# Kernel tuning notes

Measured on AMD Instinct MI355X. Metric: run time of the kernel, lower is better.

## Reference

```python
import jax, jax.numpy as jnp
import numpy as np

N_NODES = 50000
N_EDGES = 800000
D_IN, D_HID, D_OUT = 256, 128, 64
NEG_SLOPE = 0.2  # PyG GATConv default


def gat_conv(x, W, a_src, a_dst, b, src, dst, n):
    """Single-head PyG-style GATConv with self-loops already in (src, dst)."""
    h = x @ W                                  # [N, d_out]
    # per-edge attention logits: LeakyReLU(a_src . h_src + a_dst . h_dst)
    e = jax.nn.leaky_relu((h @ a_src)[src] + (h @ a_dst)[dst], NEG_SLOPE)  # [E]
    # segment softmax over incoming edges of each dst node (stable)
    e = e - jax.ops.segment_max(e, dst, num_segments=n)[dst]
    p = jnp.exp(e)
    p = p / jax.ops.segment_sum(p, dst, num_segments=n)[dst]
    # weighted scatter-add of source messages
    out = jax.ops.segment_sum(p[:, None] * h[src], dst, num_segments=n)
    return out + b


def setup_inputs() -> dict:
    key = jax.random.key(0)
    ks = jax.random.split(key, 10)
    x = jax.random.normal(ks[0], (N_NODES, D_IN), dtype=jnp.float32)
    edge_index = jax.random.randint(ks[1], (2, N_EDGES), 0, N_NODES, dtype=jnp.int32)
    s1 = 1.0 / np.sqrt(D_IN)
    s2 = 1.0 / np.sqrt(D_HID)
    W1 = jax.random.normal(ks[2], (D_IN, D_HID), dtype=jnp.float32) * s1
    a_src1 = jax.random.normal(ks[3], (D_HID,), dtype=jnp.float32) * s2
    a_dst1 = jax.random.normal(ks[4], (D_HID,), dtype=jnp.float32) * s2
    b1 = jnp.zeros((D_HID,), dtype=jnp.float32)
    W2 = jax.random.normal(ks[5], (D_HID, D_OUT), dtype=jnp.float32) * s2
    a_src2 = jax.random.normal(ks[6], (D_OUT,), dtype=jnp.float32) * (1.0 / np.sqrt(D_OUT))
    a_dst2 = jax.random.normal(ks[7], (D_OUT,), dtype=jnp.float32) * (1.0 / np.sqrt(D_OUT))
    b2 = jnp.zeros((D_OUT,), dtype=jnp.float32)
    return {"x": x, "edge_index": edge_index, "W1": W1, "a_src1": a_src1,
            "a_dst1": a_dst1, "b1": b1, "W2": W2, "a_src2": a_src2,
            "a_dst2": a_dst2, "b2": b2}


def reference(x, edge_index, W1, a_src1, a_dst1, b1, W2, a_src2, a_dst2, b2):
    n = x.shape[0]
    loops = jnp.arange(n, dtype=edge_index.dtype)
    src = jnp.concatenate([edge_index[0], loops])  # add_self_loops=True (PyG default)
    dst = jnp.concatenate([edge_index[1], loops])
    h = gat_conv(x, W1, a_src1, a_dst1, b1, src, dst, n)
    h = jax.nn.relu(h)
    return gat_conv(h, W2, a_src2, a_dst2, b2, src, dst, n)
```

## Files before the change

kernel.cpp:

```cpp
#include <hip/hip_runtime.h>
#include <stdint.h>

#define DIN 256
#define DHID 128
#define DOUTD 64
#define NBLK 128
#define BCAP 4096
#define SCAP 1024

typedef __attribute__((ext_vector_type(8))) short bf16x8;
typedef __attribute__((ext_vector_type(4))) float f32x4;

__device__ __forceinline__ uint32_t pack_bf16x2(float x, float y) {
    uint32_t ux = __builtin_bit_cast(uint32_t, x);
    uint32_t uy = __builtin_bit_cast(uint32_t, y);
    ux += 0x7fffu + ((ux >> 16) & 1u);
    uy += 0x7fffu + ((uy >> 16) & 1u);
    return (ux >> 16) | (uy & 0xffff0000u);
}
__device__ __forceinline__ uint16_t to_bf16(float x) {
    uint32_t u = __builtin_bit_cast(uint32_t, x);
    u += 0x7fffu + ((u >> 16) & 1u);
    return (uint16_t)(u >> 16);
}
__device__ __forceinline__ float bflo(uint32_t v) { return __builtin_bit_cast(float, v << 16); }
__device__ __forceinline__ float bfhi(uint32_t v) { return __builtin_bit_cast(float, v & 0xffff0000u); }

template<int K, int N>
__device__ __forceinline__ void prepack_body(
    const float* __restrict__ W, uint16_t* __restrict__ Bp, int t)
{
    constexpr int CB = N / 16;
    if (t >= (K / 32) * CB * 64) return;
    const int lane = t & 63, fi = t >> 6;
    const int c = fi % CB, kb = fi / CB;
    const int j  = 16 * c + (lane & 15);
    const int k0 = kb * 32 + (lane >> 4) * 8;
    uint32_t o[4];
    #pragma unroll
    for (int i = 0; i < 4; ++i) {
        float lo = W[(size_t)(k0 + 2 * i)     * N + j];
        float hi = W[(size_t)(k0 + 2 * i + 1) * N + j];
        o[i] = pack_bf16x2(lo, hi);
    }
    *reinterpret_cast<uint4*>(&Bp[(size_t)t * 8]) = make_uint4(o[0], o[1], o[2], o[3]);
}

__global__ __launch_bounds__(256) void prepack_both_kernel(
    const float* __restrict__ W1, uint16_t* __restrict__ Bp1,
    const float* __restrict__ W2, uint16_t* __restrict__ Bp2,
    int* __restrict__ cntG, int nbuck)
{
    if (blockIdx.x == 0) {
        for (int i = threadIdx.x; i < nbuck; i += 256) cntG[i] = 0;
    }
    if (blockIdx.x < 16)
        prepack_body<DIN, DHID>(W1, Bp1, blockIdx.x * 256 + threadIdx.x);
    else
        prepack_body<DHID, DOUTD>(W2, Bp2, (blockIdx.x - 16) * 256 + threadIdx.x);
}

template<int K, int N, bool AF32>
__device__ __forceinline__ void gemm_body(
    uint16_t* __restrict__ As,
    const void* __restrict__ A, const uint16_t* __restrict__ Bp,
    uint16_t* __restrict__ Cout, const float* __restrict__ a_s,
    const float* __restrict__ a_d, float* __restrict__ asrc,
    float* __restrict__ adst, int M, int bid)
{
    constexpr int KB = K / 32, CB = N / 16;
    const int tid = threadIdx.x;
    const int row0 = bid * 64;

    if (AF32) {
        constexpr int NIT = 64 * K / 4 / 256;
        #pragma unroll
        for (int i = 0; i < NIT; ++i) {
            int u = tid + i * 256;
            int row = u / (K / 4);
            int k4  = (u % (K / 4)) * 4;
            float4 v = make_float4(0.f, 0.f, 0.f, 0.f);
            if (row0 + row < M)
                v = *reinterpret_cast<const float4*>((const float*)A + (size_t)(row0 + row) * K + k4);
            uint32_t byte = (uint32_t)row * (K * 2) + k4 * 2;
            byte ^= (row & 7) << 4;
            *reinterpret_cast<uint2*>((char*)As + byte) =
                make_uint2(pack_bf16x2(v.x, v.y), pack_bf16x2(v.z, v.w));
        }
    } else {
        constexpr int NIT = 64 * K / 8 / 256;
        #pragma unroll
        for (int i = 0; i < NIT; ++i) {
            int u = tid + i * 256;
            int row = u / (K / 8);
            int k8  = (u % (K / 8)) * 8;
            uint4 v = make_uint4(0u, 0u, 0u, 0u);
            if (row0 + row < M)
                v = *reinterpret_cast<const uint4*>((const uint16_t*)A + (size_t)(row0 + row) * K + k8);
            uint32_t byte = (uint32_t)row * (K * 2) + k8 * 2;
            byte ^= (row & 7) << 4;
            *reinterpret_cast<uint4*>((char*)As + byte) = v;
        }
    }
    __syncthreads();

    const int w = tid >> 6, l = tid & 63;
    const int rA = w * 16 + (l & 15);

    f32x4 acc[CB] = {};
    const char* blane = (const char*)Bp + l * 16;

    #pragma unroll
    for (int kb = 0; kb < KB; ++kb) {
        uint32_t abyte = (uint32_t)rA * (K * 2) + (kb * 32 + (l >> 4) * 8) * 2;
        abyte ^= (rA & 7) << 4;
        bf16x8 a = *reinterpret_cast<const bf16x8*>((const char*)As + abyte);
        #pragma unroll
        for (int c = 0; c < CB; ++c) {
            bf16x8 b = *reinterpret_cast<const bf16x8*>(blane + (size_t)(kb * CB + c) * 1024);
            acc[c] = __builtin_amdgcn_mfma_f32_16x16x32_bf16(a, b, acc[c], 0, 0, 0);
        }
    }

    const int rb = w * 16 + (l >> 4) * 4;
    const int colb = l & 15;

    #pragma unroll
    for (int c = 0; c < CB; ++c) {
        #pragma unroll
        for (int r = 0; r < 4; ++r) {
            int grow = row0 + rb + r;
            if (grow < M)
                Cout[(size_t)grow * N + c * 16 + colb] = to_bf16(acc[c][r]);
        }
    }

    float ps[4] = {}, pd[4] = {};
    #pragma unroll
    for (int c = 0; c < CB; ++c) {
        float asv = a_s[c * 16 + colb];
        float adv = a_d[c * 16 + colb];
        #pragma unroll
        for (int r = 0; r < 4; ++r) {
            ps[r] += acc[c][r] * asv;
            pd[r] += acc[c][r] * adv;
        }
    }
    #pragma unroll
    for (int mask = 1; mask < 16; mask <<= 1) {
        #pragma unroll
        for (int r = 0; r < 4; ++r) {
            ps[r] += __shfl_xor(ps[r], mask);
            pd[r] += __shfl_xor(pd[r], mask);
        }
    }
    if (colb == 0) {
        #pragma unroll
        for (int r = 0; r < 4; ++r) {
            int grow = row0 + rb + r;
            if (grow < M) { asrc[grow] = ps[r]; adst[grow] = pd[r]; }
        }
    }
}

__global__ __launch_bounds__(256) void hybrid_kernel(
    const int* __restrict__ ei, int E, int n, int nbuck, int chunk,
    int* __restrict__ cntG, uint32_t* __restrict__ bucketed,
    const float* __restrict__ x, const uint16_t* __restrict__ Bp1,
    uint16_t* __restrict__ Hb, const float* __restrict__ a_s,
    const float* __restrict__ a_d, float* __restrict__ asrc,
    float* __restrict__ adst)
{
    __shared__ __align__(16) uint16_t As[64 * DIN];
    __shared__ int h[512];
    __shared__ int curL[512];

    if (blockIdx.x < NBLK) {
        for (int i = threadIdx.x; i < nbuck; i += 256) h[i] = 0;
        __syncthreads();
        const int blk = blockIdx.x;
        const int ET = E + n;
        const int e0 = blk * chunk, e1 = min(e0 + chunk, ET);
        for (int e = e0 + threadIdx.x; e < e1; e += 256) {
            int d = (e < E) ? ei[E + e] : (e - E);
            atomicAdd(&h[d >> 7], 1);
        }
        __syncthreads();
        for (int i = threadIdx.x; i < nbuck; i += 256) {
            int c = h[i];
            int base = i * BCAP;
            if (c) base += atomicAdd(&cntG[i], c);
            curL[i] = base;
        }
        __syncthreads();
        for (int e = e0 + threadIdx.x; e < e1; e += 256) {
            int s, d;
            if (e < E) { s = ei[e]; d = ei[E + e]; }
            else       { s = e - E; d = s; }
            int pos = atomicAdd(&curL[d >> 7], 1);
            bucketed[pos] = ((uint32_t)d << 16) | (uint32_t)s;
        }
    } else {
        gemm_body<DIN, DHID, true>(As, x, Bp1, Hb, a_s, a_d, asrc, adst, n,
                                   blockIdx.x - NBLK);
    }
}

__global__ __launch_bounds__(256) void gemm2_kernel(
    const uint16_t* __restrict__ A, const uint16_t* __restrict__ Bp,
    uint16_t* __restrict__ Cout, const float* __restrict__ a_s,
    const float* __restrict__ a_d, float* __restrict__ asrc,
    float* __restrict__ adst, int M)
{
    __shared__ __align__(16) uint16_t As[64 * DHID];
    gemm_body<DHID, DOUTD, false>(As, A, Bp, Cout, a_s, a_d, asrc, adst, M,
                                  blockIdx.x);
}

template<int D, bool RELU, bool OUTB16>
__global__ __launch_bounds__(256) void aggF_kernel(
    const uint32_t* __restrict__ bucketed, const int* __restrict__ cntG,
    const uint32_t* __restrict__ Hb, const float* __restrict__ asrc,
    const float* __restrict__ adst, const float* __restrict__ bias,
    void* __restrict__ out, int n)
{
    constexpr int C16 = D / 8;
    constexpr int EPI = 64 / C16;
    __shared__ uint16_t csr_l[SCAP];
    __shared__ int hist[32];
    __shared__ int scn[32];
    __shared__ int offs_l[32];
    __shared__ int cur[32];

    const int b     = blockIdx.x >> 2;
    const int slice = blockIdx.x & 3;
    const int tid = threadIdx.x;
    const int bbase = b * BCAP;
    const int cnt = cntG[b];

    if (tid < 32) hist[tid] = 0;
    __syncthreads();
    for (int i = tid; i < cnt; i += 256) {
        uint32_t pk = bucketed[bbase + i];
        int ln = (pk >> 16) & 127;
        if ((ln >> 5) == slice) atomicAdd(&hist[ln & 31], 1);
    }
    __syncthreads();
    if (tid < 32) scn[tid] = hist[tid];
    __syncthreads();
    #pragma unroll
    for (int off = 1; off < 32; off <<= 1) {
        int v = (tid < 32 && tid >= off) ? scn[tid - off] : 0;
        __syncthreads();
        if (tid < 32) scn[tid] += v;
        __syncthreads();
    }
    if (tid < 32) {
        int excl = scn[tid] - hist[tid];
        offs_l[tid] = excl;
        cur[tid] = excl;
    }
    __syncthreads();
    for (int i = tid; i < cnt; i += 256) {
        uint32_t pk = bucketed[bbase + i];
        int ln = (pk >> 16) & 127;
        if ((ln >> 5) == slice) {
            int pos = atomicAdd(&cur[ln & 31], 1);
            csr_l[pos] = (uint16_t)(pk & 0xFFFFu);
        }
    }
    __syncthreads();

    const int wv = tid >> 6, lane = tid & 63;
    const int seg = lane / C16;
    const int chk = lane & (C16 - 1);
    const uint4* __restrict__ H4 = reinterpret_cast<const uint4*>(Hb);

    for (int j = 0; j < 8; ++j) {
        const int ln = wv + 4 * j;
        const int node = b * 128 + slice * 32 + ln;
        if (node >= n) continue;
        const int beg = offs_l[ln];
        const int deg = hist[ln];
        const float ad = adst[node];

        float acc[8] = {};
        float ssum = 0.f;

        for (int base = 0; base < deg; base += 64) {
            const int lim = min(64, deg - base);
            float wt = 0.f; int st = 0;
            if (lane < lim) {
                st = csr_l[beg + base + lane];
                float t = asrc[st] + ad;
                t = (t > 0.f) ? t : 0.2f * t;
                wt = __expf(t);
            }
            ssum += wt;
            const int iters = (lim + 2 * EPI - 1) / (2 * EPI);
            #pragma unroll 2
            for (int it = 0; it < iters; ++it) {
                int e0 = it * 2 * EPI + seg;
                int e1 = e0 + EPI;
                float w0 = __shfl(wt, e0);
                int   s0 = __shfl(st, e0);
                float w1 = __shfl(wt, e1);
                int   s1 = __shfl(st, e1);
                uint4 v0 = H4[(size_t)s0 * (D / 8) + chk];
                uint4 v1 = H4[(size_t)s1 * (D / 8) + chk];
                acc[0] += w0 * bflo(v0.x); acc[1] += w0 * bfhi(v0.x);
                acc[2] += w0 * bflo(v0.y); acc[3] += w0 * bfhi(v0.y);
                acc[4] += w0 * bflo(v0.z); acc[5] += w0 * bfhi(v0.z);
                acc[6] += w0 * bflo(v0.w); acc[7] += w0 * bfhi(v0.w);
                acc[0] += w1 * bflo(v1.x); acc[1] += w1 * bfhi(v1.x);
                acc[2] += w1 * bflo(v1.y); acc[3] += w1 * bfhi(v1.y);
                acc[4] += w1 * bflo(v1.z); acc[5] += w1 * bfhi(v1.z);
                acc[6] += w1 * bflo(v1.w); acc[7] += w1 * bfhi(v1.w);
            }
        }

        #pragma unroll
        for (int mask = C16; mask < 64; mask <<= 1)
            #pragma unroll
            for (int q = 0; q < 8; ++q)
                acc[q] += __shfl_xor(acc[q], mask);
        #pragma unroll
        for (int off = 32; off; off >>= 1) ssum += __shfl_xor(ssum, off);
        const float inv = 1.f / ssum;

        if (seg == 0) {
            const int col0 = chk * 8;
            float r[8];
            #pragma unroll
            for (int q = 0; q < 8; ++q) {
                r[q] = acc[q] * inv + bias[col0 + q];
                if (RELU) r[q] = fmaxf(r[q], 0.f);
            }
            if (OUTB16) {
                uint4 o = make_uint4(pack_bf16x2(r[0], r[1]), pack_bf16x2(r[2], r[3]),
                                     pack_bf16x2(r[4], r[5]), pack_bf16x2(r[6], r[7]));
                *(reinterpret_cast<uint4*>(out) + (size_t)node * (D / 8) + chk) = o;
            } else {
                float* op = (float*)out + (size_t)node * D + col0;
                *reinterpret_cast<float4*>(op)     = make_float4(r[0], r[1], r[2], r[3]);
                *reinterpret_cast<float4*>(op + 4) = make_float4(r[4], r[5], r[6], r[7]);
            }
        }
    }
}

extern "C" void kernel_launch(void* const* d_in, const int* in_sizes, int n_in,
                              void* d_out, int out_size, void* d_ws, size_t ws_size,
                              hipStream_t stream)
{
    const float* x   = (const float*)d_in[0];
    const int*   ei  = (const int*)  d_in[1];
    const float* W1  = (const float*)d_in[2];
    const float* as1 = (const float*)d_in[3];
    const float* ad1 = (const float*)d_in[4];
    const float* b1  = (const float*)d_in[5];
    const float* W2  = (const float*)d_in[6];
    const float* as2 = (const float*)d_in[7];
    const float* ad2 = (const float*)d_in[8];
    const float* b2  = (const float*)d_in[9];
    float* out = (float*)d_out;

    const int n  = in_sizes[0] / DIN;
    const int E  = in_sizes[1] / 2;
    const int ET = E + n;

    const int nbuck  = (n + 127) >> 7;
    const int chunk  = (ET + NBLK - 1) / NBLK;

    char* ws = (char*)d_ws;
    size_t off = 0;
    auto alloc = [&](size_t bytes) -> void* {
        off = (off + 255) & ~(size_t)255;
        void* p = ws + off;
        off += bytes;
        return p;
    };
    uint16_t* Hb   = (uint16_t*)alloc((size_t)n * DHID * 2);
    uint16_t* O1b  = (uint16_t*)alloc((size_t)n * DHID * 2);
    uint16_t* H2b  = (uint16_t*)alloc((size_t)n * DOUTD * 2);
    float* asrc    = (float*)alloc((size_t)n * 4);
    float* adst    = (float*)alloc((size_t)n * 4);
    uint16_t* Bp1  = (uint16_t*)alloc((size_t)DIN * DHID * 2);
    uint16_t* Bp2  = (uint16_t*)alloc((size_t)DHID * DOUTD * 2);
    int* cntG  = (int*)alloc((size_t)nbuck * 4);
    uint32_t* bucketed = (uint32_t*)alloc((size_t)nbuck * BCAP * 4);

    const int ng = (n + 63) / 64;

    prepack_both_kernel<<<20, 256, 0, stream>>>(W1, Bp1, W2, Bp2, cntG, nbuck);

    hybrid_kernel<<<NBLK + ng, 256, 0, stream>>>(
        ei, E, n, nbuck, chunk, cntG, bucketed,
        x, Bp1, Hb, as1, ad1, asrc, adst);

    aggF_kernel<DHID, true, true><<<nbuck * 4, 256, 0, stream>>>(
        bucketed, cntG, (const uint32_t*)Hb, asrc, adst, b1, O1b, n);

    gemm2_kernel<<<ng, 256, 0, stream>>>(O1b, Bp2, H2b, as2, ad2, asrc, adst, n);

    aggF_kernel<DOUTD, false, false><<<nbuck * 4, 256, 0, stream>>>(
        bucketed, cntG, (const uint32_t*)H2b, asrc, adst, b2, out, n);
}
```

Before: 209.2 us.

## Fuse layer-2 GEMM into layer-1 aggregation and split hybrid bucketing/GEMM kernel

Layer-1 aggregation now keeps each block's 32 output rows in swizzled shared memory and runs the layer-2 MFMA GEMM and attention-logit projection in the same kernel. This removes the O1 intermediate round trip through global memory and one kernel launch. The former hybrid kernel, which ran edge bucketing and GEMM1 in one grid, is split into two separate sequential kernels, so the two phases no longer overlap. Layer-2 logits also get their own buffers.

```diff
diff --git a/kernel.cpp b/kernel.cpp
--- a/kernel.cpp
+++ b/kernel.cpp
@@ -163,67 +163,246 @@
     }
 }
 
-__global__ __launch_bounds__(256) void hybrid_kernel(
-    const int* __restrict__ ei, int E, int n, int nbuck, int chunk,
-    int* __restrict__ cntG, uint32_t* __restrict__ bucketed,
-    const float* __restrict__ x, const uint16_t* __restrict__ Bp1,
-    uint16_t* __restrict__ Hb, const float* __restrict__ a_s,
-    const float* __restrict__ a_d, float* __restrict__ asrc,
-    float* __restrict__ adst)
-{
-    __shared__ __align__(16) uint16_t As[64 * DIN];
-    __shared__ int h[512];
-    __shared__ int curL[512];
-
-    if (blockIdx.x < NBLK) {
-        for (int i = threadIdx.x; i < nbuck; i += 256) h[i] = 0;
-        __syncthreads();
-        const int blk = blockIdx.x;
-        const int ET = E + n;
-        const int e0 = blk * chunk, e1 = min(e0 + chunk, ET);
-        for (int e = e0 + threadIdx.x; e < e1; e += 256) {
-            int d = (e < E) ? ei[E + e] : (e - E);
-            atomicAdd(&h[d >> 7], 1);
-        }
-        __syncthreads();
-        for (int i = threadIdx.x; i < nbuck; i += 256) {
-            int c = h[i];
-            int base = i * BCAP;
-            if (c) base += atomicAdd(&cntG[i], c);
-            curL[i] = base;
-        }
-        __syncthreads();
-        for (int e = e0 + threadIdx.x; e < e1; e += 256) {
-            int s, d;
-            if (e < E) { s = ei[e]; d = ei[E + e]; }
-            else       { s = e - E; d = s; }
-            int pos = atomicAdd(&curL[d >> 7], 1);
-            bucketed[pos] = ((uint32_t)d << 16) | (uint32_t)s;
-        }
-    } else {
-        gemm_body<DIN, DHID, true>(As, x, Bp1, Hb, a_s, a_d, asrc, adst, n,
-                                   blockIdx.x - NBLK);
-    }
-}
-
-__global__ __launch_bounds__(256) void gemm2_kernel(
-    const uint16_t* __restrict__ A, const uint16_t* __restrict__ Bp,
+__global__ __launch_bounds__(256) void gemm1_kernel(
+    const float* __restrict__ A, const uint16_t* __restrict__ Bp,
     uint16_t* __restrict__ Cout, const float* __restrict__ a_s,
     const float* __restrict__ a_d, float* __restrict__ asrc,
     float* __restrict__ adst, int M)
 {
-    __shared__ __align__(16) uint16_t As[64 * DHID];
-    gemm_body<DHID, DOUTD, false>(As, A, Bp, Cout, a_s, a_d, asrc, adst, M,
-                                  blockIdx.x);
-}
-
-template<int D, bool RELU, bool OUTB16>
-__global__ __launch_bounds__(256) void aggF_kernel(
+    __shared__ __align__(16) uint16_t As[64 * DIN];
+    gemm_body<DIN, DHID, true>(As, A, Bp, Cout, a_s, a_d, asrc, adst, M, blockIdx.x);
+}
+
+__global__ __launch_bounds__(256) void histscatter_kernel(
+    const int* __restrict__ ei, int E, int n, int nbuck, int chunk,
+    int* __restrict__ cntG, uint32_t* __restrict__ bucketed)
+{
+    __shared__ int h[512];
+    __shared__ int curL[512];
+    for (int i = threadIdx.x; i < nbuck; i += 256) h[i] = 0;
+    __syncthreads();
+    const int blk = blockIdx.x;
+    const int ET = E + n;
+    const int e0 = blk * chunk, e1 = min(e0 + chunk, ET);
+    for (int e = e0 + threadIdx.x; e < e1; e += 256) {
+        int d = (e < E) ? ei[E + e] : (e - E);
+        atomicAdd(&h[d >> 7], 1);
+    }
+    __syncthreads();
+    for (int i = threadIdx.x; i < nbuck; i += 256) {
+        int c = h[i];
+        int base = i * BCAP;
+        if (c) base += atomicAdd(&cntG[i], c);
+        curL[i] = base;
+    }
+    __syncthreads();
+    for (int e = e0 + threadIdx.x; e < e1; e += 256) {
+        int s, d;
+        if (e < E) { s = ei[e]; d = ei[E + e]; }
+        else       { s = e - E; d = s; }
+        int pos = atomicAdd(&curL[d >> 7], 1);
+        bucketed[pos] = ((uint32_t)d << 16) | (uint32_t)s;
+    }
+}
+
+__global__ __launch_bounds__(256) void aggF1_fused_kernel(
+    const uint32_t* __restrict__ bucketed, const int* __restrict__ cntG,
+    const uint32_t* __restrict__ Hb, const float* __restrict__ asrc1,
+    const float* __restrict__ adst1, const float* __restrict__ b1,
+    const uint16_t* __restrict__ Bp2, const float* __restrict__ as2,
+    const float* __restrict__ ad2, uint16_t* __restrict__ H2b,
+    float* __restrict__ asrc2, float* __restrict__ adst2, int n)
+{
+    constexpr int C16 = DHID / 8;
+    constexpr int EPI = 64 / C16;
+    __shared__ uint16_t csr_l[SCAP];
+    __shared__ int hist[32];
+    __shared__ int scn[32];
+    __shared__ int offs_l[32];
+    __shared__ int cur[32];
+    __shared__ __align__(16) uint16_t O1[32 * DHID];
+    __shared__ float ps_l[32][2], pd_l[32][2];
+
+    const int b     = blockIdx.x >> 2;
+    const int slice = blockIdx.x & 3;
+    const int tid = threadIdx.x;
+    const int bbase = b * BCAP;
+    const int cnt = cntG[b];
+    const int nodebase = b * 128 + slice * 32;
+
+    if (tid < 32) hist[tid] = 0;
+    __syncthreads();
+    for (int i = tid; i < cnt; i += 256) {
+        uint32_t pk = bucketed[bbase + i];
+        int ln = (pk >> 16) & 127;
+        if ((ln >> 5) == slice) atomicAdd(&hist[ln & 31], 1);
+    }
+    __syncthreads();
+    if (tid < 32) scn[tid] = hist[tid];
+    __syncthreads();
+    #pragma unroll
+    for (int off = 1; off < 32; off <<= 1) {
+        int v = (tid < 32 && tid >= off) ? scn[tid - off] : 0;
+        __syncthreads();
+        if (tid < 32) scn[tid] += v;
+        __syncthreads();
+    }
+    if (tid < 32) {
+        int excl = scn[tid] - hist[tid];
+        offs_l[tid] = excl;
+        cur[tid] = excl;
+    }
+    __syncthreads();
+    for (int i = tid; i < cnt; i += 256) {
+        uint32_t pk = bucketed[bbase + i];
+        int ln = (pk >> 16) & 127;
+        if ((ln >> 5) == slice) {
+            int pos = atomicAdd(&cur[ln & 31], 1);
+            csr_l[pos] = (uint16_t)(pk & 0xFFFFu);
+        }
+    }
+    __syncthreads();
+
+    const int wv = tid >> 6, lane = tid & 63;
+    const int seg = lane / C16;
+    const int chk = lane & (C16 - 1);
+    const uint4* __restrict__ H4 = reinterpret_cast<const uint4*>(Hb);
+
+    for (int j = 0; j < 8; ++j) {
+        const int ln = wv + 4 * j;
+        const int node = nodebase + ln;
+        float acc[8] = {};
+        float ssum = 0.f;
+        if (node < n) {
+            const int beg = offs_l[ln];
+            const int deg = hist[ln];
+            const float ad = adst1[node];
+            for (int base = 0; base < deg; base += 64) {
+                const int lim = min(64, deg - base);
+                float wt = 0.f; int st = 0;
+                if (lane < lim) {
+                    st = csr_l[beg + base + lane];
+                    float t = asrc1[st] + ad;
+                    t = (t > 0.f) ? t : 0.2f * t;
+                    wt = __expf(t);
+                }
+                ssum += wt;
+                const int iters = (lim + 2 * EPI - 1) / (2 * EPI);
+                #pragma unroll 2
+                for (int it = 0; it < iters; ++it) {
+                    int e0 = it * 2 * EPI + seg;
+                    int e1 = e0 + EPI;
+                    float w0 = __shfl(wt, e0);
+                    int   s0 = __shfl(st, e0);
+                    float w1 = __shfl(wt, e1);
+                    int   s1 = __shfl(st, e1);
+                    uint4 v0 = H4[(size_t)s0 * C16 + chk];
+                    uint4 v1 = H4[(size_t)s1 * C16 + chk];
+                    acc[0] += w0 * bflo(v0.x); acc[1] += w0 * bfhi(v0.x);
+                    acc[2] += w0 * bflo(v0.y); acc[3] += w0 * bfhi(v0.y);
+                    acc[4] += w0 * bflo(v0.z); acc[5] += w0 * bfhi(v0.z);
+                    acc[6] += w0 * bflo(v0.w); acc[7] += w0 * bfhi(v0.w);
+                    acc[0] += w1 * bflo(v1.x); acc[1] += w1 * bfhi(v1.x);
+                    acc[2] += w1 * bflo(v1.y); acc[3] += w1 * bfhi(v1.y);
+                    acc[4] += w1 * bflo(v1.z); acc[5] += w1 * bfhi(v1.z);
+                    acc[6] += w1 * bflo(v1.w); acc[7] += w1 * bfhi(v1.w);
+                }
+            }
+            #pragma unroll
+            for (int mask = C16; mask < 64; mask <<= 1)
+                #pragma unroll
+                for (int q = 0; q < 8; ++q)
+                    acc[q] += __shfl_xor(acc[q], mask);
+            #pragma unroll
+            for (int off = 32; off; off >>= 1) ssum += __shfl_xor(ssum, off);
+        }
+        if (seg == 0) {
+            uint4 o = make_uint4(0u, 0u, 0u, 0u);
+            if (node < n) {
+                const float inv = 1.f / ssum;
+                const int col0 = chk * 8;
+                float r[8];
+                #pragma unroll
+                for (int q = 0; q < 8; ++q)
+                    r[q] = fmaxf(acc[q] * inv + b1[col0 + q], 0.f);
+                o = make_uint4(pack_bf16x2(r[0], r[1]), pack_bf16x2(r[2], r[3]),
+                               pack_bf16x2(r[4], r[5]), pack_bf16x2(r[6], r[7]));
+            }
+            uint32_t byte = (uint32_t)ln * (DHID * 2) + chk * 16;
+            byte ^= (ln & 7) << 4;
+            *reinterpret_cast<uint4*>((char*)O1 + byte) = o;
+        }
+    }
+    __syncthreads();
+
+    const int row_blk = (wv & 1) * 16;
+    const int colhalf = wv >> 1;
+    const int rA = row_blk + (lane & 15);
+    f32x4 acc2[2] = {};
+    const char* blane = (const char*)Bp2 + lane * 16;
+    #pragma unroll
+    for (int kb = 0; kb < 4; ++kb) {
+        uint32_t abyte = (uint32_t)rA * (DHID * 2) + (uint32_t)kb * 64 + (lane >> 4) * 16;
+        abyte ^= (rA & 7) << 4;
+        bf16x8 a = *reinterpret_cast<const bf16x8*>((const char*)O1 + abyte);
+        #pragma unroll
+        for (int cc = 0; cc < 2; ++cc) {
+            int c = colhalf * 2 + cc;
+            bf16x8 bb = *reinterpret_cast<const bf16x8*>(blane + (size_t)(kb * 4 + c) * 1024);
+            acc2[cc] = __builtin_amdgcn_mfma_f32_16x16x32_bf16(a, bb, acc2[cc], 0, 0, 0);
+        }
+    }
+
+    const int rb = row_blk + (lane >> 4) * 4;
+    const int colb = lane & 15;
+    float ps[4] = {}, pd[4] = {};
+    #pragma unroll
+    for (int cc = 0; cc < 2; ++cc) {
+        const int col = (colhalf * 2 + cc) * 16 + colb;
+        const float asv = as2[col];
+        const float adv = ad2[col];
+        #pragma unroll
+        for (int r = 0; r < 4; ++r) {
+            float v = acc2[cc][r];
+            int node = nodebase + rb + r;
+            if (node < n)
+                H2b[(size_t)node * DOUTD + col] = to_bf16(v);
+            ps[r] += v * asv;
+            pd[r] += v * adv;
+        }
+    }
+    #pragma unroll
+    for (int mask = 1; mask < 16; mask <<= 1) {
+        #pragma unroll
+        for (int r = 0; r < 4; ++r) {
+            ps[r] += __shfl_xor(ps[r], mask);
+            pd[r] += __shfl_xor(pd[r], mask);
+        }
+    }
+    if (colb == 0) {
+        #pragma unroll
+        for (int r = 0; r < 4; ++r) {
+            ps_l[rb + r][colhalf] = ps[r];
+            pd_l[rb + r][colhalf] = pd[r];
+        }
+    }
+    __syncthreads();
+    if (tid < 32) {
+        int node = nodebase + tid;
+        if (node < n) {
+            asrc2[node] = ps_l[tid][0] + ps_l[tid][1];
+            adst2[node] = pd_l[tid][0] + pd_l[tid][1];
+        }
+    }
+}
+
+__global__ __launch_bounds__(256) void aggF2_kernel(
     const uint32_t* __restrict__ bucketed, const int* __restrict__ cntG,
     const uint32_t* __restrict__ Hb, const float* __restrict__ asrc,
     const float* __restrict__ adst, const float* __restrict__ bias,
-    void* __restrict__ out, int n)
-{
+    float* __restrict__ out, int n)
+{
+    constexpr int D = DOUTD;
     constexpr int C16 = D / 8;
     constexpr int EPI = 64 / C16;
     __shared__ uint16_t csr_l[SCAP];
@@ -306,8 +485,8 @@
                 int   s0 = __shfl(st, e0);
                 float w1 = __shfl(wt, e1);
                 int   s1 = __shfl(st, e1);
-                uint4 v0 = H4[(size_t)s0 * (D / 8) + chk];
-                uint4 v1 = H4[(size_t)s1 * (D / 8) + chk];
+                uint4 v0 = H4[(size_t)s0 * C16 + chk];
+                uint4 v1 = H4[(size_t)s1 * C16 + chk];
                 acc[0] += w0 * bflo(v0.x); acc[1] += w0 * bfhi(v0.x);
                 acc[2] += w0 * bflo(v0.y); acc[3] += w0 * bfhi(v0.y);
                 acc[4] += w0 * bflo(v0.z); acc[5] += w0 * bfhi(v0.z);
@@ -332,19 +511,11 @@
             const int col0 = chk * 8;
             float r[8];
             #pragma unroll
-            for (int q = 0; q < 8; ++q) {
+            for (int q = 0; q < 8; ++q)
                 r[q] = acc[q] * inv + bias[col0 + q];
-                if (RELU) r[q] = fmaxf(r[q], 0.f);
-            }
-            if (OUTB16) {
-                uint4 o = make_uint4(pack_bf16x2(r[0], r[1]), pack_bf16x2(r[2], r[3]),
-                                     pack_bf16x2(r[4], r[5]), pack_bf16x2(r[6], r[7]));
-                *(reinterpret_cast<uint4*>(out) + (size_t)node * (D / 8) + chk) = o;
-            } else {
-                float* op = (float*)out + (size_t)node * D + col0;
-                *reinterpret_cast<float4*>(op)     = make_float4(r[0], r[1], r[2], r[3]);
-                *reinterpret_cast<float4*>(op + 4) = make_float4(r[4], r[5], r[6], r[7]);
-            }
+            float* op = out + (size_t)node * D + col0;
+            *reinterpret_cast<float4*>(op)     = make_float4(r[0], r[1], r[2], r[3]);
+            *reinterpret_cast<float4*>(op + 4) = make_float4(r[4], r[5], r[6], r[7]);
         }
     }
 }
@@ -381,10 +552,11 @@
         return p;
     };
     uint16_t* Hb   = (uint16_t*)alloc((size_t)n * DHID * 2);
-    uint16_t* O1b  = (uint16_t*)alloc((size_t)n * DHID * 2);
     uint16_t* H2b  = (uint16_t*)alloc((size_t)n * DOUTD * 2);
-    float* asrc    = (float*)alloc((size_t)n * 4);
-    float* adst    = (float*)alloc((size_t)n * 4);
+    float* asrc1   = (float*)alloc((size_t)n * 4);
+    float* adst1   = (float*)alloc((size_t)n * 4);
+    float* asrc2   = (float*)alloc((size_t)n * 4);
+    float* adst2   = (float*)alloc((size_t)n * 4);
     uint16_t* Bp1  = (uint16_t*)alloc((size_t)DIN * DHID * 2);
     uint16_t* Bp2  = (uint16_t*)alloc((size_t)DHID * DOUTD * 2);
     int* cntG  = (int*)alloc((size_t)nbuck * 4);
@@ -394,15 +566,14 @@
 
     prepack_both_kernel<<<20, 256, 0, stream>>>(W1, Bp1, W2, Bp2, cntG, nbuck);
 
-    hybrid_kernel<<<NBLK + ng, 256, 0, stream>>>(
-        ei, E, n, nbuck, chunk, cntG, bucketed,
-        x, Bp1, Hb, as1, ad1, asrc, adst);
-
-    aggF_kernel<DHID, true, true><<<nbuck * 4, 256, 0, stream>>>(
-        bucketed, cntG, (const uint32_t*)Hb, asrc, adst, b1, O1b, n);
-
-    gemm2_kernel<<<ng, 256, 0, stream>>>(O1b, Bp2, H2b, as2, ad2, asrc, adst, n);
-
-    aggF_kernel<DOUTD, false, false><<<nbuck * 4, 256, 0, stream>>>(
-        bucketed, cntG, (const uint32_t*)H2b, asrc, adst, b2, out, n);
-}
+    histscatter_kernel<<<NBLK, 256, 0, stream>>>(ei, E, n, nbuck, chunk, cntG, bucketed);
+
+    gemm1_kernel<<<ng, 256, 0, stream>>>(x, Bp1, Hb, as1, ad1, asrc1, adst1, n);
+
+    aggF1_fused_kernel<<<nbuck * 4, 256, 0, stream>>>(
+        bucketed, cntG, (const uint32_t*)Hb, asrc1, adst1, b1,
+        Bp2, as2, ad2, H2b, asrc2, adst2, n);
+
+    aggF2_kernel<<<nbuck * 4, 256, 0, stream>>>(
+        bucketed, cntG, (const uint32_t*)H2b, asrc2, adst2, b2, out, n);
+}
```

Result: slower. 234.8 us (+12.2%).
